# Kernel optimization log

Hardware: AMD Instinct MI355X
Metric: run time of the kernel (lower is better)

The kernel has to match this reference:

```python
import jax, jax.numpy as jnp
import numpy as np

B, N, FIN, FOUT, H = 4, 2048, 256, 256, 4
D = FOUT // H  # out_per_head


def setup_inputs() -> dict:
    key = jax.random.key(0)
    k1, k2, k3, k4 = jax.random.split(key, 4)
    h = jax.random.normal(k1, (B, N, FIN), dtype=jnp.float32)
    adj = jax.random.randint(k2, (B, N, N), 0, 2, dtype=jnp.int32)
    idx = jnp.arange(N)
    adj = adj.at[:, idx, idx].set(1)  # self-loops: avoid empty softmax rows
    W = jax.random.normal(k3, (FOUT, FIN), dtype=jnp.float32) / np.sqrt(FIN)
    attn = jax.random.normal(k4, (H, 2 * D), dtype=jnp.float32) * 0.1
    return {"h": h, "adj": adj, "W": W, "attn": attn}


def reference(h, adj, W, attn):
    Bb, Nn, _ = h.shape
    Hh = attn.shape[0]
    d = attn.shape[1] // 2
    # h_proj: [B, H, N, d]  (nn.Linear with no bias: h @ W.T)
    hp = (h @ W.T).reshape(Bb, Nn, Hh, d).transpose(0, 2, 1, 3)
    # attn . concat(h_i, h_j) == (a_src . h_i) + (a_dst . h_j); avoids O(N^2 * 2d) concat
    a_src, a_dst = attn[:, :d], attn[:, d:]
    s = jnp.einsum('bhnd,hd->bhn', hp, a_src)  # score contribution of row node i
    t = jnp.einsum('bhnd,hd->bhn', hp, a_dst)  # score contribution of col node j
    e = jax.nn.leaky_relu(s[:, :, :, None] + t[:, :, None, :], negative_slope=0.2)
    e = jnp.where(adj[:, None, :, :] != 0, e, -jnp.inf)
    alpha = jax.nn.softmax(e, axis=-1)  # [B, H, N, N]
    h_new = jnp.einsum('bhij,bhjd->bhid', alpha, hp)
    h_new = h_new.transpose(0, 2, 1, 3).reshape(Bb, Nn, Hh * d)
    return h_new, alpha.mean(axis=1)
```

## Files before the change

kernel.cpp:

```cpp
#include <hip/hip_runtime.h>
#include <math.h>

typedef unsigned long long u64;
typedef unsigned short ushort_t;
typedef float f32x4 __attribute__((ext_vector_type(4)));
typedef short short8 __attribute__((ext_vector_type(8)));

#define BB 4
#define NN 2048
#define FINE 256
#define FOUTE 256
#define HH 4
#define DD 64
#define NW 32

__device__ __forceinline__ float lrelu(float x) { return fmaxf(x, 0.2f * x); }

__device__ __forceinline__ unsigned short f2bf(float x) {
  unsigned u = __float_as_uint(x);
  unsigned r = u + 0x7FFFu + ((u >> 16) & 1u);
  return (unsigned short)(r >> 16);
}

__device__ __forceinline__ unsigned cvtpk(float lo, float hi) {
  unsigned r;
  asm("v_cvt_pk_bf16_f32 %0, %1, %2" : "=v"(r) : "v"(lo), "v"(hi));
  return r;
}

__global__ __launch_bounds__(256) void k_zero(float4* __restrict__ p) {
  p[(size_t)blockIdx.x * 256 + threadIdx.x] = make_float4(0.f, 0.f, 0.f, 0.f);
}

__global__ __launch_bounds__(256) void k_pack(const int* __restrict__ adj, u64* __restrict__ pack) {
  int row = blockIdx.x;
  int wv = threadIdx.x >> 6, ln = threadIdx.x & 63;
  const int* arow = adj + (size_t)row * NN;
  u64* prow = pack + (size_t)row * NW;
  for (int w = wv; w < NW; w += 4) {
    u64 m = __ballot(arow[(w << 6) + ln] != 0);
    if (ln == 0) prow[w] = m;
  }
}

__global__ __launch_bounds__(256) void k_gemm1(const float* __restrict__ hI, const float* __restrict__ W,
                                               const float* __restrict__ attn,
                                               ushort_t* __restrict__ hpT,
                                               float* __restrict__ sB, float* __restrict__ tB,
                                               float* __restrict__ tB4) {
  __shared__ ushort_t Ab[64 * 256];
  __shared__ ushort_t Bb[64 * 256];
  __shared__ ushort_t tT[64][72];
  int m0 = blockIdx.x * 64;
  int hh = blockIdx.y;
  int f0 = hh * 64;
  int tid = threadIdx.x;
  int w = tid >> 6, lane = tid & 63;
  int li = lane & 15, g = lane >> 4;

#pragma unroll
  for (int q = 0; q < 16; ++q) {
    int fi = (q << 8) + tid;
    int row = fi >> 6, f4 = fi & 63;
    float4 va = *(const float4*)&hI[(size_t)(m0 + row) * FINE + (f4 << 2)];
    float4 vb = *(const float4*)&W[(size_t)(f0 + row) * FINE + (f4 << 2)];
    int byteOff = (row << 9) + ((f4 << 3) ^ ((row & 7) << 4));
    *(uint2*)((char*)Ab + byteOff) = make_uint2(cvtpk(va.x, va.y), cvtpk(va.z, va.w));
    *(uint2*)((char*)Bb + byteOff) = make_uint2(cvtpk(vb.x, vb.y), cvtpk(vb.z, vb.w));
  }
  __syncthreads();

  f32x4 acc[4] = {};
  int arow = (w << 4) + li;
  int abase = arow << 9, asw = (arow & 7) << 4;
#pragma unroll
  for (int kk = 0; kk < 8; ++kk) {
    short8 a = *(const short8*)((char*)Ab + abase + (((kk << 6) + (g << 4)) ^ asw));
#pragma unroll
    for (int f = 0; f < 4; ++f) {
      int brow = (f << 4) + li;
      short8 b = *(const short8*)((char*)Bb + (brow << 9) + (((kk << 6) + (g << 4)) ^ ((brow & 7) << 4)));
      acc[f] = __builtin_amdgcn_mfma_f32_16x16x32_bf16(a, b, acc[f], 0, 0, 0);
    }
  }

  float as4[4], ad4[4];
#pragma unroll
  for (int f = 0; f < 4; ++f) {
    as4[f] = attn[(hh << 7) + (f << 4) + li];
    ad4[f] = attn[(hh << 7) + 64 + (f << 4) + li];
  }
  float ps[4] = {0.f, 0.f, 0.f, 0.f}, pt[4] = {0.f, 0.f, 0.f, 0.f};
#pragma unroll
  for (int f = 0; f < 4; ++f)
#pragma unroll
    for (int r = 0; r < 4; ++r) { ps[r] += acc[f][r] * as4[f]; pt[r] += acc[f][r] * ad4[f]; }
#pragma unroll
  for (int off = 1; off <= 8; off <<= 1) {
#pragma unroll
    for (int r = 0; r < 4; ++r) { ps[r] += __shfl_xor(ps[r], off); pt[r] += __shfl_xor(pt[r], off); }
  }
  int b0 = m0 >> 11, n0 = m0 & (NN - 1);
  if (li == 0) {
#pragma unroll
    for (int r = 0; r < 4; ++r) {
      int nn = n0 + (w << 4) + (g << 2) + r;
      size_t idx = (size_t)(b0 * HH + hh) * NN + nn;
      sB[idx] = ps[r]; tB[idx] = pt[r];
      tB4[((size_t)b0 * NN + nn) * 4 + hh] = pt[r];
    }
  }
#pragma unroll
  for (int f = 0; f < 4; ++f)
#pragma unroll
    for (int r = 0; r < 4; ++r)
      tT[(f << 4) + li][(w << 4) + (g << 2) + r] = f2bf(acc[f][r]);
  __syncthreads();
#pragma unroll
  for (int q = 0; q < 2; ++q) {
    int dr = (q << 5) + (tid >> 3);
    int seg = tid & 7;
    *(short8*)&hpT[((size_t)((b0 * HH + hh) << 6) + dr) * NN + n0 + (seg << 3)] =
        *(const short8*)&tT[dr][seg << 3];
  }
}

__global__ __launch_bounds__(256) void k_mls(const float* __restrict__ sB, const float* __restrict__ tB4,
                                             const u64* __restrict__ pack, float* __restrict__ cB,
                                             float* __restrict__ outMean) {
  __shared__ float4 t4s[2048];
  int tid = threadIdx.x;
  int lane = tid & 63;
  int bbase = blockIdx.x << 4;
  int b = bbase >> 11;
  const float4* t4 = (const float4*)tB4 + (size_t)b * NN;
#pragma unroll
  for (int q = 0; q < 8; ++q) t4s[(q << 8) + tid] = t4[(q << 8) + tid];
  __syncthreads();

  int r0 = __builtin_amdgcn_readfirstlane(bbase + ((tid >> 6) << 2));
  const u64* p0 = pack + (size_t)(r0 + 0) * NW;
  const u64* p1 = pack + (size_t)(r0 + 1) * NW;
  const u64* p2 = pack + (size_t)(r0 + 2) * NW;
  const u64* p3 = pack + (size_t)(r0 + 3) * NW;
  unsigned mr0 = 0, mr1 = 0, mr2 = 0, mr3 = 0;
  float4 tm0, tm1, tm2, tm3;
  tm0 = tm1 = tm2 = tm3 = make_float4(-1e30f, -1e30f, -1e30f, -1e30f);
#pragma unroll 4
  for (int k = 0; k < NW; ++k) {
    bool b0 = (p0[k] >> lane) & 1ull, b1 = (p1[k] >> lane) & 1ull;
    bool b2 = (p2[k] >> lane) & 1ull, b3 = (p3[k] >> lane) & 1ull;
    mr0 |= (unsigned)b0 << k; mr1 |= (unsigned)b1 << k;
    mr2 |= (unsigned)b2 << k; mr3 |= (unsigned)b3 << k;
    float4 tv = t4s[(k << 6) + lane];
    tm0.x = fmaxf(tm0.x, b0 ? tv.x : -1e30f); tm0.y = fmaxf(tm0.y, b0 ? tv.y : -1e30f);
    tm0.z = fmaxf(tm0.z, b0 ? tv.z : -1e30f); tm0.w = fmaxf(tm0.w, b0 ? tv.w : -1e30f);
    tm1.x = fmaxf(tm1.x, b1 ? tv.x : -1e30f); tm1.y = fmaxf(tm1.y, b1 ? tv.y : -1e30f);
    tm1.z = fmaxf(tm1.z, b1 ? tv.z : -1e30f); tm1.w = fmaxf(tm1.w, b1 ? tv.w : -1e30f);
    tm2.x = fmaxf(tm2.x, b2 ? tv.x : -1e30f); tm2.y = fmaxf(tm2.y, b2 ? tv.y : -1e30f);
    tm2.z = fmaxf(tm2.z, b2 ? tv.z : -1e30f); tm2.w = fmaxf(tm2.w, b2 ? tv.w : -1e30f);
    tm3.x = fmaxf(tm3.x, b3 ? tv.x : -1e30f); tm3.y = fmaxf(tm3.y, b3 ? tv.y : -1e30f);
    tm3.z = fmaxf(tm3.z, b3 ? tv.z : -1e30f); tm3.w = fmaxf(tm3.w, b3 ? tv.w : -1e30f);
  }
  float4* tms[4] = {&tm0, &tm1, &tm2, &tm3};
#pragma unroll
  for (int off = 32; off; off >>= 1) {
#pragma unroll
    for (int r = 0; r < 4; ++r) {
      float4& t = *tms[r];
      t.x = fmaxf(t.x, __shfl_xor(t.x, off));
      t.y = fmaxf(t.y, __shfl_xor(t.y, off));
      t.z = fmaxf(t.z, __shfl_xor(t.z, off));
      t.w = fmaxf(t.w, __shfl_xor(t.w, off));
    }
  }
  float sv[4][4], Ah[4][4], Bh[4][4], mh[4][4];
#pragma unroll
  for (int r = 0; r < 4; ++r) {
    float4 t = *tms[r];
    float tmv[4] = {t.x, t.y, t.z, t.w};
#pragma unroll
    for (int h = 0; h < 4; ++h) {
      float s = sB[(size_t)(b * HH + h) * NN + ((r0 + r) & (NN - 1))];
      float m = lrelu(s + tmv[h]);
      sv[r][h] = s; mh[r][h] = m; Ah[r][h] = s - m; Bh[r][h] = fmaf(0.2f, s, -m);
    }
  }
  float4 ls0, ls1, ls2, ls3;
  ls0 = ls1 = ls2 = ls3 = make_float4(0.f, 0.f, 0.f, 0.f);
#pragma unroll 2
  for (int k = 0; k < NW; ++k) {
    float4 tv = t4s[(k << 6) + lane];
    float tvv[4] = {tv.x, tv.y, tv.z, tv.w};
    bool bb[4] = {(bool)((mr0 >> k) & 1u), (bool)((mr1 >> k) & 1u),
                  (bool)((mr2 >> k) & 1u), (bool)((mr3 >> k) & 1u)};
    float4* lss[4] = {&ls0, &ls1, &ls2, &ls3};
#pragma unroll
    for (int r = 0; r < 4; ++r) {
      float* lp = &lss[r]->x;
#pragma unroll
      for (int h = 0; h < 4; ++h) {
        float e = __expf(fmaxf(tvv[h] + Ah[r][h], fmaf(0.2f, tvv[h], Bh[r][h])));
        lp[h] += bb[r] ? e : 0.0f;
      }
    }
  }
  float4* lss[4] = {&ls0, &ls1, &ls2, &ls3};
#pragma unroll
  for (int off = 32; off; off >>= 1) {
#pragma unroll
    for (int r = 0; r < 4; ++r) {
      float4& l = *lss[r];
      l.x += __shfl_xor(l.x, off); l.y += __shfl_xor(l.y, off);
      l.z += __shfl_xor(l.z, off); l.w += __shfl_xor(l.w, off);
    }
  }
  float A2[4][4], B2[4][4];
#pragma unroll
  for (int r = 0; r < 4; ++r) {
    float4 l = *lss[r];
    float lv[4] = {l.x, l.y, l.z, l.w};
#pragma unroll
    for (int h = 0; h < 4; ++h) {
      float c = mh[r][h] + __logf(lv[h]);
      A2[r][h] = sv[r][h] - c; B2[r][h] = fmaf(0.2f, sv[r][h], -c);
      if (lane == 0) cB[(size_t)(b * HH + h) * NN + ((r0 + r) & (NN - 1))] = c;
    }
  }
  unsigned mrs[4] = {mr0, mr1, mr2, mr3};
#pragma unroll 2
  for (int k = 0; k < NW; ++k) {
    float4 tv = t4s[(k << 6) + lane];
    float tvv[4] = {tv.x, tv.y, tv.z, tv.w};
#pragma unroll
    for (int r = 0; r < 4; ++r) {
      float a = 0.f;
#pragma unroll
      for (int h = 0; h < 4; ++h)
        a += __expf(fmaxf(tvv[h] + A2[r][h], fmaf(0.2f, tvv[h], B2[r][h])));
      bool bit = (mrs[r] >> k) & 1u;
      outMean[(size_t)(r0 + r) * NN + (k << 6) + lane] = bit ? 0.25f * a : 0.0f;
    }
  }
}

__global__ __launch_bounds__(256) void k_pv(const ushort_t* __restrict__ hpT,
                                            const float* __restrict__ sB, const float* __restrict__ cB,
                                            const float* __restrict__ tB, const u64* __restrict__ pack,
                                            float* __restrict__ out) {
  __shared__ ushort_t hpTile[2][4096];
  int blk = blockIdx.x;
  int jh = blockIdx.y;
  int it = blk & 31, bh = blk >> 5;
  int b = bh >> 2, hh = bh & 3;
  int i0 = it << 6;
  int tid = threadIdx.x;
  int w = tid >> 6, lane = tid & 63;
  int li = lane & 15, g = lane >> 4;
  int irow = i0 + (w << 4) + li;
  float sI = sB[(size_t)bh * NN + irow];
  float cI = cB[(size_t)bh * NN + irow];
  float A0 = sI - cI, B0 = fmaf(0.2f, sI, -cI);
  const u64* packRow = pack + ((size_t)b * NN + irow) * NW;
  const float* tRow = tB + (size_t)bh * NN;

  int drow0 = (w << 4) + (lane >> 3);
  int xslot = (lane & 7) ^ (lane >> 3);
  const ushort_t* srcBase0 = hpT + ((size_t)(bh << 6) + drow0) * NN + (xslot << 3);
  const ushort_t* srcBase1 = srcBase0 + (size_t)8 * NN;

#define STAGE(buf, j0c)                                                                        \
  do {                                                                                         \
    __builtin_amdgcn_global_load_lds(                                                          \
        (const __attribute__((address_space(1))) void*)(srcBase0 + (j0c)),                     \
        (__attribute__((address_space(3))) void*)&hpTile[buf][(w << 10)], 16, 0, 0);           \
    __builtin_amdgcn_global_load_lds(                                                          \
        (const __attribute__((address_space(1))) void*)(srcBase1 + (j0c)),                     \
        (__attribute__((address_space(3))) void*)&hpTile[buf][(w << 10) + 512], 16, 0, 0);     \
  } while (0)

  f32x4 acc[4] = {};
  int jc0 = jh << 4;
  STAGE(0, jc0 << 6);
  STAGE(1, (jc0 + 1) << 6);
  float4 ta0, ta1, tb0, tb1;
  u64 wbits;
  {
    const float4* tp4 = (const float4*)(tRow + (jc0 << 6) + (g << 3));
    ta0 = tp4[0]; ta1 = tp4[1]; tb0 = tp4[8]; tb1 = tp4[9];
    wbits = packRow[jc0];
  }
  int cur = 0;

  for (int jc = jc0; jc < jc0 + 16; ++jc) {
    float tva[8] = {ta0.x, ta0.y, ta0.z, ta0.w, ta1.x, ta1.y, ta1.z, ta1.w};
    float tvb[8] = {tb0.x, tb0.y, tb0.z, tb0.w, tb1.x, tb1.y, tb1.z, tb1.w};
    unsigned bits0 = (unsigned)(wbits >> (g << 3));
    unsigned bits1 = (unsigned)(wbits >> (32 + (g << 3)));
    float ea[8], eb[8];
#pragma unroll
    for (int jj = 0; jj < 8; ++jj) {
      float e0 = __expf(fmaxf(tva[jj] + A0, fmaf(0.2f, tva[jj], B0)));
      ea[jj] = ((bits0 >> jj) & 1u) ? e0 : 0.0f;
      float e1 = __expf(fmaxf(tvb[jj] + A0, fmaf(0.2f, tvb[jj], B0)));
      eb[jj] = ((bits1 >> jj) & 1u) ? e1 : 0.0f;
    }
    uint4 ua, ub;
    ua.x = cvtpk(ea[0], ea[1]); ua.y = cvtpk(ea[2], ea[3]);
    ua.z = cvtpk(ea[4], ea[5]); ua.w = cvtpk(ea[6], ea[7]);
    ub.x = cvtpk(eb[0], eb[1]); ub.y = cvtpk(eb[2], eb[3]);
    ub.z = cvtpk(eb[4], eb[5]); ub.w = cvtpk(eb[6], eb[7]);
    short8 a0 = __builtin_bit_cast(short8, ua);
    short8 a1 = __builtin_bit_cast(short8, ub);

    if (jc < jc0 + 15) {
      const float4* tp4 = (const float4*)(tRow + ((jc + 1) << 6) + (g << 3));
      ta0 = tp4[0]; ta1 = tp4[1]; tb0 = tp4[8]; tb1 = tp4[9];
      wbits = packRow[jc + 1];
    }

    asm volatile("" ::: "memory");
    __builtin_amdgcn_sched_barrier(0);
    __builtin_amdgcn_s_barrier();
    __builtin_amdgcn_sched_barrier(0);

    const char* tile = (const char*)hpTile[cur];
#pragma unroll
    for (int f = 0; f < 4; ++f) {
      int dr = (f << 4) + li;
      int ro = dr << 7;
      int sw = (dr & 7) << 4;
      short8 b0 = *(const short8*)(tile + ro + ((g << 4) ^ sw));
      short8 b1 = *(const short8*)(tile + ro + ((64 + (g << 4)) ^ sw));
      acc[f] = __builtin_amdgcn_mfma_f32_16x16x32_bf16(a0, b0, acc[f], 0, 0, 0);
      acc[f] = __builtin_amdgcn_mfma_f32_16x16x32_bf16(a1, b1, acc[f], 0, 0, 0);
    }

    asm volatile("s_waitcnt lgkmcnt(0)" ::: "memory");
    __builtin_amdgcn_sched_barrier(0);
    __builtin_amdgcn_s_barrier();

    if (jc + 2 < jc0 + 16) STAGE(cur, (jc + 2) << 6);
    cur ^= 1;
  }
#undef STAGE

#pragma unroll
  for (int f = 0; f < 4; ++f)
#pragma unroll
    for (int r = 0; r < 4; ++r) {
      int i = i0 + (w << 4) + (g << 2) + r;
      int d = (f << 4) + li;
      atomicAdd(&out[((size_t)(b * NN + i)) * FOUTE + (hh << 6) + d], acc[f][r]);
    }
}

extern "C" void kernel_launch(void* const* d_in, const int* in_sizes, int n_in,
                              void* d_out, int out_size, void* d_ws, size_t ws_size,
                              hipStream_t stream) {
  const float* hIn  = (const float*)d_in[0];
  const int*   adj  = (const int*)d_in[1];
  const float* W    = (const float*)d_in[2];
  const float* attn = (const float*)d_in[3];
  float* out = (float*)d_out;
  float* outMean = out + (size_t)BB * NN * FOUTE;

  ushort_t* hpT = (ushort_t*)d_ws;
  float* sB  = (float*)(hpT + (size_t)BB * HH * DD * NN);
  float* tB  = sB + BB * HH * NN;
  float* cB  = tB + BB * HH * NN;
  float* tB4 = cB + BB * HH * NN;
  u64* pack  = (u64*)(tB4 + BB * HH * NN);

  hipLaunchKernelGGL(k_zero,  dim3((BB * NN * FOUTE) / (4 * 256)), dim3(256), 0, stream, (float4*)out);
  hipLaunchKernelGGL(k_pack,  dim3(BB * NN), dim3(256), 0, stream, adj, pack);
  hipLaunchKernelGGL(k_gemm1, dim3((BB * NN) / 64, HH), dim3(256), 0, stream, hIn, W, attn, hpT, sB, tB, tB4);
  hipLaunchKernelGGL(k_mls,   dim3((BB * NN) / 16), dim3(256), 0, stream, sB, tB4, pack, cB, outMean);
  hipLaunchKernelGGL(k_pv,    dim3(BB * HH * (NN / 64), 2), dim3(256), 0, stream, hpT, sB, cB, tB, pack, out);
}
```

Before: 112.2 us.

## Use global column max as softmax shift and halve rows per wave in k_mls

The row-softmax shift now uses the unmasked maximum of t over all columns, computed once per block with a cross-wave reduction, instead of a masked per-row max. This removes one full masked pass over the adjacency bits, so the sum of exponentials is accumulated in the same loop that builds the mask bits. Each wave now handles 2 rows instead of 4 and the grid doubles, which trades more blocks and repeated t-tile loads for lower register use. The looser shift is still an upper bound, but it could underflow rows whose neighbours all have small t.

Result: faster. 106.1 us (-5.5%).

```diff
diff --git a/kernel.cpp b/kernel.cpp
--- a/kernel.cpp
+++ b/kernel.cpp
@@ -129,118 +129,100 @@
                                              const u64* __restrict__ pack, float* __restrict__ cB,
                                              float* __restrict__ outMean) {
   __shared__ float4 t4s[2048];
+  __shared__ float4 wpart[4];
   int tid = threadIdx.x;
   int lane = tid & 63;
-  int bbase = blockIdx.x << 4;
+  int wv = tid >> 6;
+  int bbase = blockIdx.x << 3;
   int b = bbase >> 11;
   const float4* t4 = (const float4*)tB4 + (size_t)b * NN;
 #pragma unroll
   for (int q = 0; q < 8; ++q) t4s[(q << 8) + tid] = t4[(q << 8) + tid];
   __syncthreads();
 
-  int r0 = __builtin_amdgcn_readfirstlane(bbase + ((tid >> 6) << 2));
+  float4 pm = make_float4(-1e30f, -1e30f, -1e30f, -1e30f);
+#pragma unroll
+  for (int q = 0; q < 8; ++q) {
+    float4 tv = t4s[(wv << 9) + (q << 6) + lane];
+    pm.x = fmaxf(pm.x, tv.x); pm.y = fmaxf(pm.y, tv.y);
+    pm.z = fmaxf(pm.z, tv.z); pm.w = fmaxf(pm.w, tv.w);
+  }
+#pragma unroll
+  for (int off = 32; off; off >>= 1) {
+    pm.x = fmaxf(pm.x, __shfl_xor(pm.x, off));
+    pm.y = fmaxf(pm.y, __shfl_xor(pm.y, off));
+    pm.z = fmaxf(pm.z, __shfl_xor(pm.z, off));
+    pm.w = fmaxf(pm.w, __shfl_xor(pm.w, off));
+  }
+  if (lane == 0) wpart[wv] = pm;
+  __syncthreads();
+  float4 q0 = wpart[0], q1 = wpart[1], q2 = wpart[2], q3 = wpart[3];
+  float tmax[4] = {fmaxf(fmaxf(q0.x, q1.x), fmaxf(q2.x, q3.x)),
+                   fmaxf(fmaxf(q0.y, q1.y), fmaxf(q2.y, q3.y)),
+                   fmaxf(fmaxf(q0.z, q1.z), fmaxf(q2.z, q3.z)),
+                   fmaxf(fmaxf(q0.w, q1.w), fmaxf(q2.w, q3.w))};
+
+  int r0 = __builtin_amdgcn_readfirstlane(bbase + (wv << 1));
   const u64* p0 = pack + (size_t)(r0 + 0) * NW;
   const u64* p1 = pack + (size_t)(r0 + 1) * NW;
-  const u64* p2 = pack + (size_t)(r0 + 2) * NW;
-  const u64* p3 = pack + (size_t)(r0 + 3) * NW;
-  unsigned mr0 = 0, mr1 = 0, mr2 = 0, mr3 = 0;
-  float4 tm0, tm1, tm2, tm3;
-  tm0 = tm1 = tm2 = tm3 = make_float4(-1e30f, -1e30f, -1e30f, -1e30f);
+  float sv[2][4], Ah[2][4], Bh[2][4], mh[2][4];
+#pragma unroll
+  for (int r = 0; r < 2; ++r)
+#pragma unroll
+    for (int h = 0; h < 4; ++h) {
+      float s = sB[(size_t)(b * HH + h) * NN + ((r0 + r) & (NN - 1))];
+      float m = lrelu(s + tmax[h]);
+      sv[r][h] = s; mh[r][h] = m; Ah[r][h] = s - m; Bh[r][h] = fmaf(0.2f, s, -m);
+    }
+  unsigned mr0 = 0, mr1 = 0;
+  float4 ls0 = make_float4(0.f, 0.f, 0.f, 0.f), ls1 = ls0;
 #pragma unroll 4
   for (int k = 0; k < NW; ++k) {
     bool b0 = (p0[k] >> lane) & 1ull, b1 = (p1[k] >> lane) & 1ull;
-    bool b2 = (p2[k] >> lane) & 1ull, b3 = (p3[k] >> lane) & 1ull;
     mr0 |= (unsigned)b0 << k; mr1 |= (unsigned)b1 << k;
-    mr2 |= (unsigned)b2 << k; mr3 |= (unsigned)b3 << k;
     float4 tv = t4s[(k << 6) + lane];
-    tm0.x = fmaxf(tm0.x, b0 ? tv.x : -1e30f); tm0.y = fmaxf(tm0.y, b0 ? tv.y : -1e30f);
-    tm0.z = fmaxf(tm0.z, b0 ? tv.z : -1e30f); tm0.w = fmaxf(tm0.w, b0 ? tv.w : -1e30f);
-    tm1.x = fmaxf(tm1.x, b1 ? tv.x : -1e30f); tm1.y = fmaxf(tm1.y, b1 ? tv.y : -1e30f);
-    tm1.z = fmaxf(tm1.z, b1 ? tv.z : -1e30f); tm1.w = fmaxf(tm1.w, b1 ? tv.w : -1e30f);
-    tm2.x = fmaxf(tm2.x, b2 ? tv.x : -1e30f); tm2.y = fmaxf(tm2.y, b2 ? tv.y : -1e30f);
-    tm2.z = fmaxf(tm2.z, b2 ? tv.z : -1e30f); tm2.w = fmaxf(tm2.w, b2 ? tv.w : -1e30f);
-    tm3.x = fmaxf(tm3.x, b3 ? tv.x : -1e30f); tm3.y = fmaxf(tm3.y, b3 ? tv.y : -1e30f);
-    tm3.z = fmaxf(tm3.z, b3 ? tv.z : -1e30f); tm3.w = fmaxf(tm3.w, b3 ? tv.w : -1e30f);
-  }
-  float4* tms[4] = {&tm0, &tm1, &tm2, &tm3};
+    ls0.x += b0 ? __expf(fmaxf(tv.x + Ah[0][0], fmaf(0.2f, tv.x, Bh[0][0]))) : 0.f;
+    ls0.y += b0 ? __expf(fmaxf(tv.y + Ah[0][1], fmaf(0.2f, tv.y, Bh[0][1]))) : 0.f;
+    ls0.z += b0 ? __expf(fmaxf(tv.z + Ah[0][2], fmaf(0.2f, tv.z, Bh[0][2]))) : 0.f;
+    ls0.w += b0 ? __expf(fmaxf(tv.w + Ah[0][3], fmaf(0.2f, tv.w, Bh[0][3]))) : 0.f;
+    ls1.x += b1 ? __expf(fmaxf(tv.x + Ah[1][0], fmaf(0.2f, tv.x, Bh[1][0]))) : 0.f;
+    ls1.y += b1 ? __expf(fmaxf(tv.y + Ah[1][1], fmaf(0.2f, tv.y, Bh[1][1]))) : 0.f;
+    ls1.z += b1 ? __expf(fmaxf(tv.z + Ah[1][2], fmaf(0.2f, tv.z, Bh[1][2]))) : 0.f;
+    ls1.w += b1 ? __expf(fmaxf(tv.w + Ah[1][3], fmaf(0.2f, tv.w, Bh[1][3]))) : 0.f;
+  }
 #pragma unroll
   for (int off = 32; off; off >>= 1) {
-#pragma unroll
-    for (int r = 0; r < 4; ++r) {
-      float4& t = *tms[r];
-      t.x = fmaxf(t.x, __shfl_xor(t.x, off));
-      t.y = fmaxf(t.y, __shfl_xor(t.y, off));
-      t.z = fmaxf(t.z, __shfl_xor(t.z, off));
-      t.w = fmaxf(t.w, __shfl_xor(t.w, off));
-    }
-  }
-  float sv[4][4], Ah[4][4], Bh[4][4], mh[4][4];
-#pragma unroll
-  for (int r = 0; r < 4; ++r) {
-    float4 t = *tms[r];
-    float tmv[4] = {t.x, t.y, t.z, t.w};
-#pragma unroll
-    for (int h = 0; h < 4; ++h) {
-      float s = sB[(size_t)(b * HH + h) * NN + ((r0 + r) & (NN - 1))];
-      float m = lrelu(s + tmv[h]);
-      sv[r][h] = s; mh[r][h] = m; Ah[r][h] = s - m; Bh[r][h] = fmaf(0.2f, s, -m);
-    }
-  }
-  float4 ls0, ls1, ls2, ls3;
-  ls0 = ls1 = ls2 = ls3 = make_float4(0.f, 0.f, 0.f, 0.f);
+    ls0.x += __shfl_xor(ls0.x, off); ls0.y += __shfl_xor(ls0.y, off);
+    ls0.z += __shfl_xor(ls0.z, off); ls0.w += __shfl_xor(ls0.w, off);
+    ls1.x += __shfl_xor(ls1.x, off); ls1.y += __shfl_xor(ls1.y, off);
+    ls1.z += __shfl_xor(ls1.z, off); ls1.w += __shfl_xor(ls1.w, off);
+  }
+  float A2[2][4], B2[2][4];
+  float lv0[4] = {ls0.x, ls0.y, ls0.z, ls0.w};
+  float lv1[4] = {ls1.x, ls1.y, ls1.z, ls1.w};
+#pragma unroll
+  for (int h = 0; h < 4; ++h) {
+    float c0 = mh[0][h] + __logf(lv0[h]);
+    float c1 = mh[1][h] + __logf(lv1[h]);
+    A2[0][h] = sv[0][h] - c0; B2[0][h] = fmaf(0.2f, sv[0][h], -c0);
+    A2[1][h] = sv[1][h] - c1; B2[1][h] = fmaf(0.2f, sv[1][h], -c1);
+    if (lane == 0) {
+      cB[(size_t)(b * HH + h) * NN + ((r0 + 0) & (NN - 1))] = c0;
+      cB[(size_t)(b * HH + h) * NN + ((r0 + 1) & (NN - 1))] = c1;
+    }
+  }
 #pragma unroll 2
   for (int k = 0; k < NW; ++k) {
     float4 tv = t4s[(k << 6) + lane];
     float tvv[4] = {tv.x, tv.y, tv.z, tv.w};
-    bool bb[4] = {(bool)((mr0 >> k) & 1u), (bool)((mr1 >> k) & 1u),
-                  (bool)((mr2 >> k) & 1u), (bool)((mr3 >> k) & 1u)};
-    float4* lss[4] = {&ls0, &ls1, &ls2, &ls3};
-#pragma unroll
-    for (int r = 0; r < 4; ++r) {
-      float* lp = &lss[r]->x;
-#pragma unroll
-      for (int h = 0; h < 4; ++h) {
-        float e = __expf(fmaxf(tvv[h] + Ah[r][h], fmaf(0.2f, tvv[h], Bh[r][h])));
-        lp[h] += bb[r] ? e : 0.0f;
-      }
-    }
-  }
-  float4* lss[4] = {&ls0, &ls1, &ls2, &ls3};
-#pragma unroll
-  for (int off = 32; off; off >>= 1) {
-#pragma unroll
-    for (int r = 0; r < 4; ++r) {
-      float4& l = *lss[r];
-      l.x += __shfl_xor(l.x, off); l.y += __shfl_xor(l.y, off);
-      l.z += __shfl_xor(l.z, off); l.w += __shfl_xor(l.w, off);
-    }
-  }
-  float A2[4][4], B2[4][4];
-#pragma unroll
-  for (int r = 0; r < 4; ++r) {
-    float4 l = *lss[r];
-    float lv[4] = {l.x, l.y, l.z, l.w};
+    float a0 = 0.f, a1 = 0.f;
 #pragma unroll
     for (int h = 0; h < 4; ++h) {
-      float c = mh[r][h] + __logf(lv[h]);
-      A2[r][h] = sv[r][h] - c; B2[r][h] = fmaf(0.2f, sv[r][h], -c);
-      if (lane == 0) cB[(size_t)(b * HH + h) * NN + ((r0 + r) & (NN - 1))] = c;
-    }
-  }
-  unsigned mrs[4] = {mr0, mr1, mr2, mr3};
-#pragma unroll 2
-  for (int k = 0; k < NW; ++k) {
-    float4 tv = t4s[(k << 6) + lane];
-    float tvv[4] = {tv.x, tv.y, tv.z, tv.w};
-#pragma unroll
-    for (int r = 0; r < 4; ++r) {
-      float a = 0.f;
-#pragma unroll
-      for (int h = 0; h < 4; ++h)
-        a += __expf(fmaxf(tvv[h] + A2[r][h], fmaf(0.2f, tvv[h], B2[r][h])));
-      bool bit = (mrs[r] >> k) & 1u;
-      outMean[(size_t)(r0 + r) * NN + (k << 6) + lane] = bit ? 0.25f * a : 0.0f;
-    }
+      a0 += __expf(fmaxf(tvv[h] + A2[0][h], fmaf(0.2f, tvv[h], B2[0][h])));
+      a1 += __expf(fmaxf(tvv[h] + A2[1][h], fmaf(0.2f, tvv[h], B2[1][h])));
+    }
+    outMean[(size_t)(r0 + 0) * NN + (k << 6) + lane] = ((mr0 >> k) & 1u) ? 0.25f * a0 : 0.0f;
+    outMean[(size_t)(r0 + 1) * NN + (k << 6) + lane] = ((mr1 >> k) & 1u) ? 0.25f * a1 : 0.0f;
   }
 }
 
@@ -375,6 +357,6 @@
   hipLaunchKernelGGL(k_zero,  dim3((BB * NN * FOUTE) / (4 * 256)), dim3(256), 0, stream, (float4*)out);
   hipLaunchKernelGGL(k_pack,  dim3(BB * NN), dim3(256), 0, stream, adj, pack);
   hipLaunchKernelGGL(k_gemm1, dim3((BB * NN) / 64, HH), dim3(256), 0, stream, hIn, W, attn, hpT, sB, tB, tB4);
-  hipLaunchKernelGGL(k_mls,   dim3((BB * NN) / 16), dim3(256), 0, stream, sB, tB4, pack, cB, outMean);
+  hipLaunchKernelGGL(k_mls,   dim3((BB * NN) / 8), dim3(256), 0, stream, sB, tB4, pack, cB, outMean);
   hipLaunchKernelGGL(k_pv,    dim3(BB * HH * (NN / 64), 2), dim3(256), 0, stream, hpT, sB, cB, tB, pack, out);
 }
```
